# Performance work log

Hardware: AMD Instinct MI355X
Metric: run time of the kernel (lower is better)

The kernel has to match this reference:

```python
import jax, jax.numpy as jnp
import numpy as np

IN_DIM = 256
QK_DIM = 64

def setup_inputs() -> dict:
    key = jax.random.key(0)
    ks = jax.random.split(key, 7)
    b, c, h, w = 16, IN_DIM, 96, 96
    x = jax.random.normal(ks[0], (b, c, h, w), dtype=jnp.float32)
    sc = 1.0 / np.sqrt(c)
    Wq = jax.random.normal(ks[1], (QK_DIM, c), dtype=jnp.float32) * sc
    bq = jax.random.normal(ks[2], (QK_DIM,), dtype=jnp.float32) * 0.01
    Wk = jax.random.normal(ks[3], (QK_DIM, c), dtype=jnp.float32) * sc
    bk = jax.random.normal(ks[4], (QK_DIM,), dtype=jnp.float32) * 0.01
    Wv = jax.random.normal(ks[5], (c, c), dtype=jnp.float32) * sc
    bv = jax.random.normal(ks[6], (c,), dtype=jnp.float32) * 0.01
    gamma = jnp.zeros((1,), dtype=jnp.float32) + 0.5  # nonzero so output depends on attention
    return {"x": x, "Wq": Wq, "bq": bq, "Wk": Wk, "bk": bk, "Wv": Wv, "bv": bv, "gamma": gamma}

def reference(x, Wq, bq, Wk, bk, Wv, bv, gamma):
    # 1x1-conv projections: (b,c,h,w) -> (b,q,h,w)
    Q = jnp.einsum('bchw,qc->bqhw', x, Wq) + bq[None, :, None, None]
    K = jnp.einsum('bchw,qc->bqhw', x, Wk) + bk[None, :, None, None]
    V = jnp.einsum('bchw,vc->bvhw', x, Wv) + bv[None, :, None, None]
    # column attention over height h, per (batch, width) column; unscaled scores
    scores = jnp.einsum('bqhw,bqgw->bwhg', Q, K)        # (b, w, h, h)
    attn = jax.nn.softmax(scores, axis=-1)
    # out[:, :, i] = sum_j V[:, :, j] * attn[i, j]  (bmm with attn transposed)
    out = jnp.einsum('bcgw,bwhg->bchw', V, attn)
    return gamma[0] * out + x
```

## Files before the change

kernel.cpp:

```cpp
#include <hip/hip_runtime.h>
#include <stdint.h>

#define DI __device__ __forceinline__

typedef __attribute__((ext_vector_type(4))) float f4;
typedef __attribute__((ext_vector_type(4))) float f32x4;
typedef __attribute__((ext_vector_type(2))) float f32x2;
typedef _Float16 f16;
typedef __attribute__((ext_vector_type(8))) f16 f16x8;

static constexpr int BATCH = 16, C = 256, H = 96, W = 96, QK = 64, F = 384;
static constexpr int P = H * W;

static constexpr size_t SZ_XT = (size_t)BATCH * P * C * 2;
static constexpr size_t OFF_XT = 0;
static constexpr size_t OFF_WC = OFF_XT + SZ_XT;
static constexpr size_t OFF_BC = OFF_WC + (size_t)F * C * 2;
static constexpr size_t OFF_QP = OFF_BC + 4096;
static constexpr size_t OFF_KP = OFF_QP + (size_t)BATCH * P * QK * 2;
static constexpr size_t OFF_VP = OFF_KP + (size_t)BATCH * P * QK * 2;
static constexpr size_t OFF_O1 = OFF_VP + (size_t)BATCH * P * C * 2;
static constexpr size_t WS_END = OFF_O1 + (size_t)BATCH * P * C * 2;

DI void gll16(const void* g, void* l) {
  __builtin_amdgcn_global_load_lds((const __attribute__((address_space(1))) void*)g,
                                   (__attribute__((address_space(3))) void*)l, 16, 0, 0);
}
DI f32x4 mfma16(f16x8 a, f16x8 b, f32x4 c) {
  return __builtin_amdgcn_mfma_f32_16x16x32_f16(a, b, c, 0, 0, 0);
}

__global__ __launch_bounds__(256) void wprep_kernel(
    const float* __restrict__ Wq, const float* __restrict__ bq,
    const float* __restrict__ Wk, const float* __restrict__ bk,
    const float* __restrict__ Wv, const float* __restrict__ bv,
    f16* __restrict__ Wc, float* __restrict__ bc) {
  const int f = blockIdx.x, t = threadIdx.x;
  const float* src; int row;
  if (f < 64)       { src = Wq; row = f; }
  else if (f < 128) { src = Wk; row = f - 64; }
  else              { src = Wv; row = f - 128; }
  Wc[f * C + t] = (f16)src[row * C + t];
  if (t == 0) bc[f] = (f < 64) ? bq[f] : (f < 128) ? bk[f - 64] : bv[f - 128];
}

__global__ __launch_bounds__(256) void prep_kernel(const float* __restrict__ x,
                                                   f16* __restrict__ xT) {
  __shared__ float t[64][65];
  const int b = blockIdx.z, c0 = blockIdx.y * 64, p0 = blockIdx.x * 64;
  const int tid = threadIdx.x;
  const float* xb = x + ((size_t)b * C + c0) * P + p0;
#pragma unroll
  for (int pass = 0; pass < 4; ++pass) {
    int cl = pass * 16 + (tid >> 4);
    int p4 = (tid & 15) * 4;
    f4 v = *reinterpret_cast<const f4*>(xb + (size_t)cl * P + p4);
#pragma unroll
    for (int i = 0; i < 4; ++i) t[cl][p4 + i] = v[i];
  }
  __syncthreads();
#pragma unroll
  for (int pass = 0; pass < 2; ++pass) {
    int pl = pass * 32 + (tid >> 3);
    int c8 = (tid & 7) * 8;
    f16x8 hv;
#pragma unroll
    for (int i = 0; i < 8; ++i) hv[i] = (f16)t[c8 + i][pl];
    *reinterpret_cast<f16x8*>(xT + ((size_t)b * P + p0 + pl) * C + c0 + c8) = hv;
  }
}

__global__ __launch_bounds__(256, 2) void gemm_qkv(
    const f16* __restrict__ xT, const f16* __restrict__ Wc, const float* __restrict__ bc,
    f16* __restrict__ Qp, f16* __restrict__ Kp, f16* __restrict__ Vp) {
  __shared__ f16 As[2][128 * 64];
  __shared__ f16 Bs[2][128 * 64];
  const int tid = threadIdx.x, lane = tid & 63, wv = tid >> 6;
  const int wm = wv >> 1, wn = wv & 1;
  const int c2 = ((blockIdx.x & 7) * 432) + (blockIdx.x >> 3);
  const int b = c2 / 216;
  const int r = c2 % 216;
  const int mt = r / 3, nt = r % 3;
  const int m0 = mt * 128, f0 = nt * 128;
  const f16* Ab = xT + ((size_t)b * P + m0) * C;
  const f16* Bb = Wc + (size_t)f0 * C;

  const int grow = lane >> 3;
  const int lblk = (lane & 7) ^ grow;

  f32x4 acc[4][4];
#pragma unroll
  for (int i = 0; i < 4; ++i)
#pragma unroll
    for (int j = 0; j < 4; ++j) acc[i][j] = (f32x4){0.f, 0.f, 0.f, 0.f};

  auto stage = [&](int k0, int bsel) {
#pragma unroll
    for (int s = 0; s < 4; ++s) {
      int rbase = wv * 32 + s * 8;
      int row = rbase + grow;
      gll16(Ab + (size_t)row * C + k0 + lblk * 8, &As[bsel][rbase * 64]);
      gll16(Bb + (size_t)row * C + k0 + lblk * 8, &Bs[bsel][rbase * 64]);
    }
  };
  auto compute = [&](int bsel) {
#pragma unroll
    for (int ks = 0; ks < 2; ++ks) {
      const int kb = ks * 4 + (lane >> 4);
      f16x8 a[4], bb[4];
#pragma unroll
      for (int i = 0; i < 4; ++i) {
        int row = wm * 64 + i * 16 + (lane & 15);
        a[i] = *reinterpret_cast<const f16x8*>(&As[bsel][row * 64 + ((kb ^ (row & 7)) << 3)]);
      }
#pragma unroll
      for (int j = 0; j < 4; ++j) {
        int row = wn * 64 + j * 16 + (lane & 15);
        bb[j] = *reinterpret_cast<const f16x8*>(&Bs[bsel][row * 64 + ((kb ^ (row & 7)) << 3)]);
      }
#pragma unroll
      for (int i = 0; i < 4; ++i)
#pragma unroll
        for (int j = 0; j < 4; ++j) acc[i][j] = mfma16(a[i], bb[j], acc[i][j]);
    }
  };

  stage(0, 0);
  __syncthreads();
  int buf = 0;
#pragma unroll
  for (int t = 0; t < 3; ++t) {
    stage((t + 1) * 64, buf ^ 1);
    compute(buf);
    __syncthreads();
    buf ^= 1;
  }
  compute(buf);

#pragma unroll
  for (int j = 0; j < 4; ++j) {
    const int fl = wn * 64 + j * 16 + (lane & 15);
    const float bias = bc[f0 + fl];
#pragma unroll
    for (int i = 0; i < 4; ++i) {
#pragma unroll
      for (int q = 0; q < 4; ++q) {
        int p = m0 + wm * 64 + i * 16 + ((lane >> 4) << 2) + q;
        float v = acc[i][j][q] + bias;
        if (nt == 0) {
          if (fl < 64) Qp[((size_t)b * P + p) * QK + fl] = (f16)v;
          else         Kp[((size_t)b * P + p) * QK + (fl - 64)] = (f16)v;
        } else {
          Vp[((size_t)b * P + p) * C + (nt - 1) * 128 + fl] = (f16)v;
        }
      }
    }
  }
}

__global__ __launch_bounds__(256, 1) void attn_kernel(
    const f16* __restrict__ Qp, const f16* __restrict__ Kp, const f16* __restrict__ Vp,
    f16* __restrict__ O1) {
  __shared__ char smem[12288 + 12288 + 38400 + 65536 + 384];
  f16*   qs   = (f16*)smem;
  f16*   ksm  = (f16*)(smem + 12288);
  float* sS   = (float*)(smem + 24576);
  f16*   vt   = (f16*)(smem + 24576 + 38400);
  float* rsum = (float*)(smem + 24576 + 38400 + 65536);
  f16*   sP   = (f16*)smem;

  const int tid = threadIdx.x, lane = tid & 63, wv = tid >> 6;
  const int id = ((blockIdx.x & 7) * 192) + (blockIdx.x >> 3);
  const int b = id / 96, w = id % 96;

  const int cc = tid;
  f16 vv[96];
#pragma unroll
  for (int g = 0; g < 96; ++g)
    vv[g] = Vp[((size_t)b * P + g * 96 + w) * C + cc];

  {
    const int grow = lane >> 3;
    const int lblk = (lane & 7) ^ grow;
#pragma unroll
    for (int s = 0; s < 3; ++s) {
      int sec = wv * 3 + s;
      int row = sec * 8 + grow;
      size_t src = ((size_t)b * P + (size_t)row * 96 + w) * QK + lblk * 8;
      gll16(Qp + src, &qs[sec * 512]);
      gll16(Kp + src, &ksm[sec * 512]);
    }
  }
#pragma unroll
  for (int ob = 0; ob < 12; ++ob) {
    f16x8 pk;
#pragma unroll
    for (int e = 0; e < 8; ++e) pk[e] = vv[ob * 8 + e];
    *reinterpret_cast<f16x8*>(&vt[cc * 128 + ((ob ^ (cc & 15)) << 3)]) = pk;
  }
  __syncthreads();

  {
    const int wmq = wv >> 1, wnq = wv & 1;
    f32x4 acc[3][3];
#pragma unroll
    for (int i = 0; i < 3; ++i)
#pragma unroll
      for (int j = 0; j < 3; ++j) acc[i][j] = (f32x4){0.f, 0.f, 0.f, 0.f};
#pragma unroll
    for (int ks = 0; ks < 2; ++ks) {
      const int kb = ks * 4 + (lane >> 4);
      f16x8 a[3], bb[3];
#pragma unroll
      for (int i = 0; i < 3; ++i) {
        int row = wmq * 48 + i * 16 + (lane & 15);
        a[i] = *reinterpret_cast<const f16x8*>(&qs[row * 64 + ((kb ^ (row & 7)) << 3)]);
      }
#pragma unroll
      for (int j = 0; j < 3; ++j) {
        int row = wnq * 48 + j * 16 + (lane & 15);
        bb[j] = *reinterpret_cast<const f16x8*>(&ksm[row * 64 + ((kb ^ (row & 7)) << 3)]);
      }
#pragma unroll
      for (int i = 0; i < 3; ++i)
#pragma unroll
        for (int j = 0; j < 3; ++j) acc[i][j] = mfma16(a[i], bb[j], acc[i][j]);
    }
#pragma unroll
    for (int i = 0; i < 3; ++i)
#pragma unroll
      for (int j = 0; j < 3; ++j)
#pragma unroll
        for (int q = 0; q < 4; ++q)
          sS[(wmq * 48 + i * 16 + ((lane >> 4) << 2) + q) * 100 +
             wnq * 48 + j * 16 + (lane & 15)] = acc[i][j][q];
  }
  __syncthreads();

  {
    const int grp = tid >> 4, l16 = tid & 15;
#pragma unroll
    for (int rr = 0; rr < 6; ++rr) {
      const int row = grp * 6 + rr;
      f32x2 v[3];
      float m = -1e30f;
#pragma unroll
      for (int j = 0; j < 3; ++j) {
        v[j] = *reinterpret_cast<const f32x2*>(&sS[row * 100 + 2 * l16 + 32 * j]);
        m = fmaxf(m, fmaxf(v[j][0], v[j][1]));
      }
#pragma unroll
      for (int o = 8; o >= 1; o >>= 1) m = fmaxf(m, __shfl_xor(m, o, 64));
      float e = 0.f;
#pragma unroll
      for (int j = 0; j < 3; ++j) {
        float p0 = __expf(v[j][0] - m), p1 = __expf(v[j][1] - m);
        e += p0 + p1;
        union { unsigned u; f16 h[2]; } pk;
        pk.h[0] = (f16)p0; pk.h[1] = (f16)p1;
        const int gb = (l16 >> 2) + 4 * j;
        *reinterpret_cast<unsigned*>(
            &sP[row * 128 + ((gb ^ (row & 7)) << 3) + 2 * (l16 & 3)]) = pk.u;
      }
#pragma unroll
      for (int o = 8; o >= 1; o >>= 1) e += __shfl_xor(e, o, 64);
      if (l16 == 0) rsum[row] = 1.0f / e;
    }
  }
  __syncthreads();

  {
    const int wmq = wv >> 1, wnq = wv & 1;
    f32x4 acc[3][8];
#pragma unroll
    for (int i = 0; i < 3; ++i)
#pragma unroll
      for (int j = 0; j < 8; ++j) acc[i][j] = (f32x4){0.f, 0.f, 0.f, 0.f};
#pragma unroll
    for (int ks = 0; ks < 3; ++ks) {
      const int gb = ks * 4 + (lane >> 4);
      f16x8 a[3];
#pragma unroll
      for (int i = 0; i < 3; ++i) {
        int row = wmq * 48 + i * 16 + (lane & 15);
        a[i] = *reinterpret_cast<const f16x8*>(&sP[row * 128 + ((gb ^ (row & 7)) << 3)]);
      }
#pragma unroll
      for (int j = 0; j < 8; ++j) {
        int crow = wnq * 128 + j * 16 + (lane & 15);
        f16x8 bv = *reinterpret_cast<const f16x8*>(&vt[crow * 128 + ((gb ^ (crow & 15)) << 3)]);
#pragma unroll
        for (int i = 0; i < 3; ++i) acc[i][j] = mfma16(a[i], bv, acc[i][j]);
      }
    }
    f16* ob = O1 + ((size_t)b * 96 + w) * 96 * C;
#pragma unroll
    for (int i = 0; i < 3; ++i) {
#pragma unroll
      for (int q = 0; q < 4; ++q) {
        const int h = wmq * 48 + i * 16 + ((lane >> 4) << 2) + q;
        const float rs = rsum[h];
#pragma unroll
        for (int j = 0; j < 8; ++j) {
          int c = wnq * 128 + j * 16 + (lane & 15);
          ob[(size_t)h * C + c] = (f16)(acc[i][j][q] * rs);
        }
      }
    }
  }
}

__global__ __launch_bounds__(256, 3) void epi_kernel(
    const f16* __restrict__ O1, const float* __restrict__ x,
    const float* __restrict__ gamma, float* __restrict__ out) {
  __shared__ f16 t[96 * 256];
  const int id = ((blockIdx.x & 7) * 192) + (blockIdx.x >> 3);
  const int b = id / 96, h = id % 96;
  const int tid = threadIdx.x, lane = tid & 63, wv = tid >> 6;
  {
    const int grow = lane >> 5;
#pragma unroll
    for (int s = 0; s < 12; ++s) {
      int sec = wv * 12 + s;
      int row = sec * 2 + grow;
      int lblk = (lane & 31) ^ (row & 31);
      gll16(O1 + (((size_t)b * 96 + row) * 96 + h) * C + lblk * 8, &t[sec * 512]);
    }
  }
  __syncthreads();
  const float g = gamma[0];
#pragma unroll
  for (int pass = 0; pass < 24; ++pass) {
    const int idx = pass * 256 + tid;
    const int c = idx / 24, wc = idx % 24;
    const int w4 = wc * 4;
    size_t o = (((size_t)b * C + c) * H + h) * W + w4;
    f4 xv = *reinterpret_cast<const f4*>(x + o);
    f4 r;
#pragma unroll
    for (int u = 0; u < 4; ++u) {
      int wr = w4 + u;
      f16 hv = t[wr * 256 + (((c >> 3) ^ (wr & 31)) << 3) + (c & 7)];
      r[u] = g * (float)hv + xv[u];
    }
    *reinterpret_cast<f4*>(out + o) = r;
  }
}

extern "C" void kernel_launch(void* const* d_in, const int* in_sizes, int n_in,
                              void* d_out, int out_size, void* d_ws, size_t ws_size,
                              hipStream_t stream) {
  const float* x     = (const float*)d_in[0];
  const float* Wq    = (const float*)d_in[1];
  const float* bq    = (const float*)d_in[2];
  const float* Wk    = (const float*)d_in[3];
  const float* bk    = (const float*)d_in[4];
  const float* Wv    = (const float*)d_in[5];
  const float* bv    = (const float*)d_in[6];
  const float* gamma = (const float*)d_in[7];
  float* out = (float*)d_out;
  char* ws = (char*)d_ws;
  if (ws_size < WS_END) return;

  f16*   xT = (f16*)(ws + OFF_XT);
  f16*   Wc = (f16*)(ws + OFF_WC);
  float* bc = (float*)(ws + OFF_BC);
  f16*   Qp = (f16*)(ws + OFF_QP);
  f16*   Kp = (f16*)(ws + OFF_KP);
  f16*   Vp = (f16*)(ws + OFF_VP);
  f16*   O1 = (f16*)(ws + OFF_O1);

  wprep_kernel<<<dim3(F), dim3(256), 0, stream>>>(Wq, bq, Wk, bk, Wv, bv, Wc, bc);
  prep_kernel<<<dim3(P / 64, C / 64, BATCH), dim3(256), 0, stream>>>(x, xT);
  gemm_qkv<<<dim3(3456), dim3(256), 0, stream>>>(xT, Wc, bc, Qp, Kp, Vp);
  attn_kernel<<<dim3(BATCH * 96), dim3(256), 0, stream>>>(Qp, Kp, Vp, O1);
  epi_kernel<<<dim3(BATCH * 96), dim3(256), 0, stream>>>(O1, x, gamma, out);
}
```

Measured before the change: 458.5 us.

## Fuse x transpose into QKV GEMM and restructure attention softmax in registers

Removes the separate prep kernel that wrote an fp16 transposed copy of x: the QKV GEMM now loads fp32 x directly through registers, converts it to fp16 and writes a padded LDS tile, while B still uses direct-to-LDS loads. The attention kernel does softmax on the MFMA accumulators with cross-wave max/sum reductions in place of an fp32 score buffer in LDS. V^T is stored with a 104-element stride and a mod-13 rotation to cut LDS use, and launch bounds go to 2 blocks per CU. This saves a full intermediate write and read of x and raises attention occupancy, at the cost of strided scalar global loads in the GEMM and extra index arithmetic.

```diff
diff --git a/kernel.cpp b/kernel.cpp
--- a/kernel.cpp
+++ b/kernel.cpp
@@ -5,16 +5,13 @@
 
 typedef __attribute__((ext_vector_type(4))) float f4;
 typedef __attribute__((ext_vector_type(4))) float f32x4;
-typedef __attribute__((ext_vector_type(2))) float f32x2;
 typedef _Float16 f16;
 typedef __attribute__((ext_vector_type(8))) f16 f16x8;
 
 static constexpr int BATCH = 16, C = 256, H = 96, W = 96, QK = 64, F = 384;
 static constexpr int P = H * W;
 
-static constexpr size_t SZ_XT = (size_t)BATCH * P * C * 2;
-static constexpr size_t OFF_XT = 0;
-static constexpr size_t OFF_WC = OFF_XT + SZ_XT;
+static constexpr size_t OFF_WC = 0;
 static constexpr size_t OFF_BC = OFF_WC + (size_t)F * C * 2;
 static constexpr size_t OFF_QP = OFF_BC + 4096;
 static constexpr size_t OFF_KP = OFF_QP + (size_t)BATCH * P * QK * 2;
@@ -28,6 +25,9 @@
 }
 DI f32x4 mfma16(f16x8 a, f16x8 b, f32x4 c) {
   return __builtin_amdgcn_mfma_f32_16x16x32_f16(a, b, c, 0, 0, 0);
+}
+DI int mod13(int v) {
+  return v - 13 * ((v * 5042) >> 16);
 }
 
 __global__ __launch_bounds__(256) void wprep_kernel(
@@ -44,49 +44,23 @@
   if (t == 0) bc[f] = (f < 64) ? bq[f] : (f < 128) ? bk[f - 64] : bv[f - 128];
 }
 
-__global__ __launch_bounds__(256) void prep_kernel(const float* __restrict__ x,
-                                                   f16* __restrict__ xT) {
-  __shared__ float t[64][65];
-  const int b = blockIdx.z, c0 = blockIdx.y * 64, p0 = blockIdx.x * 64;
-  const int tid = threadIdx.x;
-  const float* xb = x + ((size_t)b * C + c0) * P + p0;
-#pragma unroll
-  for (int pass = 0; pass < 4; ++pass) {
-    int cl = pass * 16 + (tid >> 4);
-    int p4 = (tid & 15) * 4;
-    f4 v = *reinterpret_cast<const f4*>(xb + (size_t)cl * P + p4);
-#pragma unroll
-    for (int i = 0; i < 4; ++i) t[cl][p4 + i] = v[i];
-  }
-  __syncthreads();
-#pragma unroll
-  for (int pass = 0; pass < 2; ++pass) {
-    int pl = pass * 32 + (tid >> 3);
-    int c8 = (tid & 7) * 8;
-    f16x8 hv;
-#pragma unroll
-    for (int i = 0; i < 8; ++i) hv[i] = (f16)t[c8 + i][pl];
-    *reinterpret_cast<f16x8*>(xT + ((size_t)b * P + p0 + pl) * C + c0 + c8) = hv;
-  }
-}
-
 __global__ __launch_bounds__(256, 2) void gemm_qkv(
-    const f16* __restrict__ xT, const f16* __restrict__ Wc, const float* __restrict__ bc,
+    const float* __restrict__ x, const f16* __restrict__ Wc, const float* __restrict__ bc,
     f16* __restrict__ Qp, f16* __restrict__ Kp, f16* __restrict__ Vp) {
-  __shared__ f16 As[2][128 * 64];
+  __shared__ f16 As[2][128 * 72];
   __shared__ f16 Bs[2][128 * 64];
   const int tid = threadIdx.x, lane = tid & 63, wv = tid >> 6;
   const int wm = wv >> 1, wn = wv & 1;
   const int c2 = ((blockIdx.x & 7) * 432) + (blockIdx.x >> 3);
-  const int b = c2 / 216;
-  const int r = c2 % 216;
+  const int b = c2 / 216, r = c2 % 216;
   const int mt = r / 3, nt = r % 3;
   const int m0 = mt * 128, f0 = nt * 128;
-  const f16* Ab = xT + ((size_t)b * P + m0) * C;
+  const float* Ax = x + (size_t)b * C * P + m0;
   const f16* Bb = Wc + (size_t)f0 * C;
 
-  const int grow = lane >> 3;
-  const int lblk = (lane & 7) ^ grow;
+  const int ap = tid & 127;
+  const int ach = tid >> 7;
+  const int grow = lane >> 3, lblk = (lane & 7) ^ grow;
 
   f32x4 acc[4][4];
 #pragma unroll
@@ -94,13 +68,30 @@
 #pragma unroll
     for (int j = 0; j < 4; ++j) acc[i][j] = (f32x4){0.f, 0.f, 0.f, 0.f};
 
-  auto stage = [&](int k0, int bsel) {
+  float av[4][8];
+  auto loadA = [&](int k0) {
 #pragma unroll
     for (int s = 0; s < 4; ++s) {
-      int rbase = wv * 32 + s * 8;
-      int row = rbase + grow;
-      gll16(Ab + (size_t)row * C + k0 + lblk * 8, &As[bsel][rbase * 64]);
-      gll16(Bb + (size_t)row * C + k0 + lblk * 8, &Bs[bsel][rbase * 64]);
+      const int c = k0 + (s * 2 + ach) * 8;
+#pragma unroll
+      for (int u = 0; u < 8; ++u) av[s][u] = Ax[(size_t)(c + u) * P + ap];
+    }
+  };
+  auto writeA = [&](int bsel) {
+#pragma unroll
+    for (int s = 0; s < 4; ++s) {
+      const int cb = s * 2 + ach;
+      f16x8 hv;
+#pragma unroll
+      for (int u = 0; u < 8; ++u) hv[u] = (f16)av[s][u];
+      *reinterpret_cast<f16x8*>(&As[bsel][ap * 72 + cb * 8]) = hv;
+    }
+  };
+  auto stageB = [&](int k0, int bsel) {
+#pragma unroll
+    for (int s = 0; s < 4; ++s) {
+      const int rbase = wv * 32 + s * 8;
+      gll16(Bb + (size_t)(rbase + grow) * C + k0 + lblk * 8, &Bs[bsel][rbase * 64]);
     }
   };
   auto compute = [&](int bsel) {
@@ -110,12 +101,12 @@
       f16x8 a[4], bb[4];
 #pragma unroll
       for (int i = 0; i < 4; ++i) {
-        int row = wm * 64 + i * 16 + (lane & 15);
-        a[i] = *reinterpret_cast<const f16x8*>(&As[bsel][row * 64 + ((kb ^ (row & 7)) << 3)]);
+        const int row = wm * 64 + i * 16 + (lane & 15);
+        a[i] = *reinterpret_cast<const f16x8*>(&As[bsel][row * 72 + kb * 8]);
       }
 #pragma unroll
       for (int j = 0; j < 4; ++j) {
-        int row = wn * 64 + j * 16 + (lane & 15);
+        const int row = wn * 64 + j * 16 + (lane & 15);
         bb[j] = *reinterpret_cast<const f16x8*>(&Bs[bsel][row * 64 + ((kb ^ (row & 7)) << 3)]);
       }
 #pragma unroll
@@ -125,13 +116,17 @@
     }
   };
 
-  stage(0, 0);
+  loadA(0);
+  stageB(0, 0);
+  writeA(0);
   __syncthreads();
   int buf = 0;
 #pragma unroll
   for (int t = 0; t < 3; ++t) {
-    stage((t + 1) * 64, buf ^ 1);
+    loadA((t + 1) * 64);
+    stageB((t + 1) * 64, buf ^ 1);
     compute(buf);
+    writeA(buf ^ 1);
     __syncthreads();
     buf ^= 1;
   }
@@ -145,8 +140,8 @@
     for (int i = 0; i < 4; ++i) {
 #pragma unroll
       for (int q = 0; q < 4; ++q) {
-        int p = m0 + wm * 64 + i * 16 + ((lane >> 4) << 2) + q;
-        float v = acc[i][j][q] + bias;
+        const int p = m0 + wm * 64 + i * 16 + ((lane >> 4) << 2) + q;
+        const float v = acc[i][j][q] + bias;
         if (nt == 0) {
           if (fl < 64) Qp[((size_t)b * P + p) * QK + fl] = (f16)v;
           else         Kp[((size_t)b * P + p) * QK + (fl - 64)] = (f16)v;
@@ -158,18 +153,19 @@
   }
 }
 
-__global__ __launch_bounds__(256, 1) void attn_kernel(
+__global__ __launch_bounds__(256, 2) void attn_kernel(
     const f16* __restrict__ Qp, const f16* __restrict__ Kp, const f16* __restrict__ Vp,
     f16* __restrict__ O1) {
-  __shared__ char smem[12288 + 12288 + 38400 + 65536 + 384];
+  __shared__ char smem[24576 + 53248 + 768 + 768];
   f16*   qs   = (f16*)smem;
   f16*   ksm  = (f16*)(smem + 12288);
-  float* sS   = (float*)(smem + 24576);
-  f16*   vt   = (f16*)(smem + 24576 + 38400);
-  float* rsum = (float*)(smem + 24576 + 38400 + 65536);
   f16*   sP   = (f16*)smem;
+  f16*   vt   = (f16*)(smem + 24576);
+  float* redm = (float*)(smem + 24576 + 53248);
+  float* reds = redm + 192;
 
   const int tid = threadIdx.x, lane = tid & 63, wv = tid >> 6;
+  const int wmq = wv >> 1, wnq = wv & 1;
   const int id = ((blockIdx.x & 7) * 192) + (blockIdx.x >> 3);
   const int b = id / 96, w = id % 96;
 
@@ -184,126 +180,129 @@
     const int lblk = (lane & 7) ^ grow;
 #pragma unroll
     for (int s = 0; s < 3; ++s) {
-      int sec = wv * 3 + s;
-      int row = sec * 8 + grow;
-      size_t src = ((size_t)b * P + (size_t)row * 96 + w) * QK + lblk * 8;
+      const int sec = wv * 3 + s;
+      const int row = sec * 8 + grow;
+      const size_t src = ((size_t)b * P + (size_t)row * 96 + w) * QK + lblk * 8;
       gll16(Qp + src, &qs[sec * 512]);
       gll16(Kp + src, &ksm[sec * 512]);
     }
   }
-#pragma unroll
-  for (int ob = 0; ob < 12; ++ob) {
-    f16x8 pk;
-#pragma unroll
-    for (int e = 0; e < 8; ++e) pk[e] = vv[ob * 8 + e];
-    *reinterpret_cast<f16x8*>(&vt[cc * 128 + ((ob ^ (cc & 15)) << 3)]) = pk;
-  }
-  __syncthreads();
-
   {
-    const int wmq = wv >> 1, wnq = wv & 1;
-    f32x4 acc[3][3];
+    const int r13 = mod13(cc);
+#pragma unroll
+    for (int ob = 0; ob < 12; ++ob) {
+      int phys = ob + r13;
+      if (phys >= 13) phys -= 13;
+      f16x8 pk;
+#pragma unroll
+      for (int e = 0; e < 8; ++e) pk[e] = vv[ob * 8 + e];
+      *reinterpret_cast<f16x8*>(&vt[cc * 104 + phys * 8]) = pk;
+    }
+  }
+  __syncthreads();
+
+  f32x4 acc[3][3];
+#pragma unroll
+  for (int i = 0; i < 3; ++i)
+#pragma unroll
+    for (int j = 0; j < 3; ++j) acc[i][j] = (f32x4){0.f, 0.f, 0.f, 0.f};
+#pragma unroll
+  for (int ks = 0; ks < 2; ++ks) {
+    const int kb = ks * 4 + (lane >> 4);
+    f16x8 a[3], bb[3];
+#pragma unroll
+    for (int i = 0; i < 3; ++i) {
+      const int row = wmq * 48 + i * 16 + (lane & 15);
+      a[i] = *reinterpret_cast<const f16x8*>(&qs[row * 64 + ((kb ^ (row & 7)) << 3)]);
+    }
+#pragma unroll
+    for (int j = 0; j < 3; ++j) {
+      const int row = wnq * 48 + j * 16 + (lane & 15);
+      bb[j] = *reinterpret_cast<const f16x8*>(&ksm[row * 64 + ((kb ^ (row & 7)) << 3)]);
+    }
 #pragma unroll
     for (int i = 0; i < 3; ++i)
 #pragma unroll
-      for (int j = 0; j < 3; ++j) acc[i][j] = (f32x4){0.f, 0.f, 0.f, 0.f};
-#pragma unroll
-    for (int ks = 0; ks < 2; ++ks) {
-      const int kb = ks * 4 + (lane >> 4);
-      f16x8 a[3], bb[3];
-#pragma unroll
-      for (int i = 0; i < 3; ++i) {
-        int row = wmq * 48 + i * 16 + (lane & 15);
-        a[i] = *reinterpret_cast<const f16x8*>(&qs[row * 64 + ((kb ^ (row & 7)) << 3)]);
-      }
+      for (int j = 0; j < 3; ++j) acc[i][j] = mfma16(a[i], bb[j], acc[i][j]);
+  }
+
+#pragma unroll
+  for (int i = 0; i < 3; ++i)
+#pragma unroll
+    for (int q = 0; q < 4; ++q) {
+      float m = fmaxf(fmaxf(acc[i][0][q], acc[i][1][q]), acc[i][2][q]);
+#pragma unroll
+      for (int o = 8; o >= 1; o >>= 1) m = fmaxf(m, __shfl_xor(m, o, 64));
+      if ((lane & 15) == 0)
+        redm[wnq * 96 + wmq * 48 + i * 16 + ((lane >> 4) << 2) + q] = m;
+    }
+  __syncthreads();
+#pragma unroll
+  for (int i = 0; i < 3; ++i)
+#pragma unroll
+    for (int q = 0; q < 4; ++q) {
+      const int h = wmq * 48 + i * 16 + ((lane >> 4) << 2) + q;
+      const float m = fmaxf(redm[h], redm[96 + h]);
+      float s = 0.f;
 #pragma unroll
       for (int j = 0; j < 3; ++j) {
-        int row = wnq * 48 + j * 16 + (lane & 15);
-        bb[j] = *reinterpret_cast<const f16x8*>(&ksm[row * 64 + ((kb ^ (row & 7)) << 3)]);
-      }
-#pragma unroll
-      for (int i = 0; i < 3; ++i)
-#pragma unroll
-        for (int j = 0; j < 3; ++j) acc[i][j] = mfma16(a[i], bb[j], acc[i][j]);
-    }
+        const float p = __expf(acc[i][j][q] - m);
+        acc[i][j][q] = p;
+        s += p;
+      }
+#pragma unroll
+      for (int o = 8; o >= 1; o >>= 1) s += __shfl_xor(s, o, 64);
+      if ((lane & 15) == 0) reds[wnq * 96 + h] = s;
+    }
+#pragma unroll
+  for (int i = 0; i < 3; ++i)
+#pragma unroll
+    for (int q = 0; q < 4; ++q) {
+      const int h = wmq * 48 + i * 16 + ((lane >> 4) << 2) + q;
+#pragma unroll
+      for (int j = 0; j < 3; ++j) {
+        const int g = wnq * 48 + j * 16 + (lane & 15);
+        sP[h * 128 + (((g >> 3) ^ (h & 7)) << 3) + (g & 7)] = (f16)acc[i][j][q];
+      }
+    }
+  __syncthreads();
+
+  {
+    f32x4 o[3][8];
 #pragma unroll
     for (int i = 0; i < 3; ++i)
 #pragma unroll
-      for (int j = 0; j < 3; ++j)
-#pragma unroll
-        for (int q = 0; q < 4; ++q)
-          sS[(wmq * 48 + i * 16 + ((lane >> 4) << 2) + q) * 100 +
-             wnq * 48 + j * 16 + (lane & 15)] = acc[i][j][q];
-  }
-  __syncthreads();
-
-  {
-    const int grp = tid >> 4, l16 = tid & 15;
-#pragma unroll
-    for (int rr = 0; rr < 6; ++rr) {
-      const int row = grp * 6 + rr;
-      f32x2 v[3];
-      float m = -1e30f;
-#pragma unroll
-      for (int j = 0; j < 3; ++j) {
-        v[j] = *reinterpret_cast<const f32x2*>(&sS[row * 100 + 2 * l16 + 32 * j]);
-        m = fmaxf(m, fmaxf(v[j][0], v[j][1]));
-      }
-#pragma unroll
-      for (int o = 8; o >= 1; o >>= 1) m = fmaxf(m, __shfl_xor(m, o, 64));
-      float e = 0.f;
-#pragma unroll
-      for (int j = 0; j < 3; ++j) {
-        float p0 = __expf(v[j][0] - m), p1 = __expf(v[j][1] - m);
-        e += p0 + p1;
-        union { unsigned u; f16 h[2]; } pk;
-        pk.h[0] = (f16)p0; pk.h[1] = (f16)p1;
-        const int gb = (l16 >> 2) + 4 * j;
-        *reinterpret_cast<unsigned*>(
-            &sP[row * 128 + ((gb ^ (row & 7)) << 3) + 2 * (l16 & 3)]) = pk.u;
-      }
-#pragma unroll
-      for (int o = 8; o >= 1; o >>= 1) e += __shfl_xor(e, o, 64);
-      if (l16 == 0) rsum[row] = 1.0f / e;
-    }
-  }
-  __syncthreads();
-
-  {
-    const int wmq = wv >> 1, wnq = wv & 1;
-    f32x4 acc[3][8];
-#pragma unroll
-    for (int i = 0; i < 3; ++i)
-#pragma unroll
-      for (int j = 0; j < 8; ++j) acc[i][j] = (f32x4){0.f, 0.f, 0.f, 0.f};
+      for (int j = 0; j < 8; ++j) o[i][j] = (f32x4){0.f, 0.f, 0.f, 0.f};
 #pragma unroll
     for (int ks = 0; ks < 3; ++ks) {
       const int gb = ks * 4 + (lane >> 4);
       f16x8 a[3];
 #pragma unroll
       for (int i = 0; i < 3; ++i) {
-        int row = wmq * 48 + i * 16 + (lane & 15);
+        const int row = wmq * 48 + i * 16 + (lane & 15);
         a[i] = *reinterpret_cast<const f16x8*>(&sP[row * 128 + ((gb ^ (row & 7)) << 3)]);
       }
 #pragma unroll
       for (int j = 0; j < 8; ++j) {
-        int crow = wnq * 128 + j * 16 + (lane & 15);
-        f16x8 bv = *reinterpret_cast<const f16x8*>(&vt[crow * 128 + ((gb ^ (crow & 15)) << 3)]);
-#pragma unroll
-        for (int i = 0; i < 3; ++i) acc[i][j] = mfma16(a[i], bv, acc[i][j]);
-      }
-    }
-    f16* ob = O1 + ((size_t)b * 96 + w) * 96 * C;
+        const int crow = wnq * 128 + j * 16 + (lane & 15);
+        int phys = gb + mod13(crow);
+        if (phys >= 13) phys -= 13;
+        const f16x8 bv = *reinterpret_cast<const f16x8*>(&vt[crow * 104 + phys * 8]);
+#pragma unroll
+        for (int i = 0; i < 3; ++i) o[i][j] = mfma16(a[i], bv, o[i][j]);
+      }
+    }
+    f16* ob_ = O1 + ((size_t)b * 96 + w) * 96 * C;
 #pragma unroll
     for (int i = 0; i < 3; ++i) {
 #pragma unroll
       for (int q = 0; q < 4; ++q) {
         const int h = wmq * 48 + i * 16 + ((lane >> 4) << 2) + q;
-        const float rs = rsum[h];
+        const float rs = 1.0f / (reds[h] + reds[96 + h]);
 #pragma unroll
         for (int j = 0; j < 8; ++j) {
-          int c = wnq * 128 + j * 16 + (lane & 15);
-          ob[(size_t)h * C + c] = (f16)(acc[i][j][q] * rs);
+          const int c = wnq * 128 + j * 16 + (lane & 15);
+          ob_[(size_t)h * C + c] = (f16)(o[i][j][q] * rs);
         }
       }
     }
@@ -321,9 +320,9 @@
     const int grow = lane >> 5;
 #pragma unroll
     for (int s = 0; s < 12; ++s) {
-      int sec = wv * 12 + s;
-      int row = sec * 2 + grow;
-      int lblk = (lane & 31) ^ (row & 31);
+      const int sec = wv * 12 + s;
+      const int row = sec * 2 + grow;
+      const int lblk = (lane & 31) ^ (row & 31);
       gll16(O1 + (((size_t)b * 96 + row) * 96 + h) * C + lblk * 8, &t[sec * 512]);
     }
   }
@@ -334,13 +333,13 @@
     const int idx = pass * 256 + tid;
     const int c = idx / 24, wc = idx % 24;
     const int w4 = wc * 4;
-    size_t o = (((size_t)b * C + c) * H + h) * W + w4;
-    f4 xv = *reinterpret_cast<const f4*>(x + o);
+    const size_t o = (((size_t)b * C + c) * H + h) * W + w4;
+    const f4 xv = *reinterpret_cast<const f4*>(x + o);
     f4 r;
 #pragma unroll
     for (int u = 0; u < 4; ++u) {
-      int wr = w4 + u;
-      f16 hv = t[wr * 256 + (((c >> 3) ^ (wr & 31)) << 3) + (c & 7)];
+      const int wr = w4 + u;
+      const f16 hv = t[wr * 256 + (((c >> 3) ^ (wr & 31)) << 3) + (c & 7)];
       r[u] = g * (float)hv + xv[u];
     }
     *reinterpret_cast<f4*>(out + o) = r;
@@ -362,7 +361,6 @@
   char* ws = (char*)d_ws;
   if (ws_size < WS_END) return;
 
-  f16*   xT = (f16*)(ws + OFF_XT);
   f16*   Wc = (f16*)(ws + OFF_WC);
   float* bc = (float*)(ws + OFF_BC);
   f16*   Qp = (f16*)(ws + OFF_QP);
@@ -371,8 +369,7 @@
   f16*   O1 = (f16*)(ws + OFF_O1);
 
   wprep_kernel<<<dim3(F), dim3(256), 0, stream>>>(Wq, bq, Wk, bk, Wv, bv, Wc, bc);
-  prep_kernel<<<dim3(P / 64, C / 64, BATCH), dim3(256), 0, stream>>>(x, xT);
-  gemm_qkv<<<dim3(3456), dim3(256), 0, stream>>>(xT, Wc, bc, Qp, Kp, Vp);
+  gemm_qkv<<<dim3(3456), dim3(256), 0, stream>>>(x, Wc, bc, Qp, Kp, Vp);
   attn_kernel<<<dim3(BATCH * 96), dim3(256), 0, stream>>>(Qp, Kp, Vp, O1);
   epi_kernel<<<dim3(BATCH * 96), dim3(256), 0, stream>>>(O1, x, gamma, out);
 }
```

Result: faster. 425.0 us (-7.3%).
